# Performance work log

Hardware: AMD Instinct MI355X
Metric: run time of the kernel (lower is better)

## Reference

```python
import jax, jax.numpy as jnp
import numpy as np

MAX_DISP = 4  # max_displacement
PAD = MAX_DISP
ODIM = 2 * MAX_DISP + 1  # 9 -> 81 cost-volume channels


def setup_inputs() -> dict:
    key = jax.random.key(0)
    k1, k2 = jax.random.split(key)
    B, C, H, W = 4, 256, 96, 192
    x1 = jax.random.normal(k1, (B, C, H, W), dtype=jnp.float32)
    x2 = jax.random.normal(k2, (B, C, H, W), dtype=jnp.float32)
    return {"x1": x1, "x2": x2}


def reference(x1, x2):
    B, C, H, W = x1.shape
    # zero-pad x2 spatially by PAD on each side (matches F.pad([pad]*4))
    x2p = jnp.pad(x2, ((0, 0), (0, 0), (PAD, PAD), (PAD, PAD)))
    cv = []
    for i in range(ODIM):          # fixed 9x9 displacement grid
        for j in range(ODIM):
            shifted = jax.lax.dynamic_slice(
                x2p, (0, 0, i, j), (B, C, H, W))
            # mean over channel dim -> [B, H, W]
            cv.append(jnp.mean(x1 * shifted, axis=1))
    return jnp.stack(cv, axis=1)  # [B, 81, H, W]
```

## Files before the change

### kernel.cpp

```cpp
#include <hip/hip_runtime.h>
#include <stddef.h>


#define NB 4
#define NC 256
#define HH 96
#define WW 192
#define TW 16
#define TH 4
#define KC 32
#define NROWS 12
#define CHW (HH * WW)
#define KSTRIDE (KC * CHW)
#define NTASK 1152

#define KS 264
#define RS 1096
#define XBI(row, kg, n) ((row) * RS + (kg) * KS + (n) * 8)

typedef __attribute__((ext_vector_type(8))) short bf16x8;
typedef __attribute__((ext_vector_type(4))) float f32x4;

__device__ __forceinline__ unsigned short f2bf(float f) {
    union { float f; unsigned u; } c; c.f = f;
    unsigned r = c.u + 0x7FFFu + ((c.u >> 16) & 1u);
    return (unsigned short)(r >> 16);
}

__global__ __launch_bounds__(512, 4) void corr_mfma(
    const float* __restrict__ x1, const float* __restrict__ x2,
    float* __restrict__ out)
{
    __shared__ union {
        unsigned short xb[NROWS * RS];
        float band[TH][9][9][18];
    } lds;

    const int lin = blockIdx.x;
    const int sw  = (lin & 7) * 144 + (lin >> 3);
    const int b   = sw / 288;
    const int t2  = sw - b * 288;
    const int ty  = t2 / 12;
    const int tx  = t2 - ty * 12;

    const int tid  = threadIdx.x;
    const int wv   = tid >> 6;
    const int lane = tid & 63;
    const int col  = lane & 15;
    const int q    = lane >> 4;
    const int r    = wv & 3;
    const int dig  = wv >> 2;
    const int w0   = tx * TW;
    const int h0   = ty * TH;
    const int h    = h0 + r;

    f32x4 acc[9];
#pragma unroll
    for (int s = 0; s < 9; ++s) acc[s] = (f32x4)0.0f;

    unsigned o2k[3];
    int      lofk[3];
    bool     okk[3];
    bool     act[3];
#pragma unroll
    for (int k = 0; k < 3; ++k) {
        const int t   = tid + k * 512;
        act[k] = (t < NTASK);
        const int seg = t % 6;
        const int u   = t / 6;
        const int cp  = u & 15;
        const int row = u >> 4;
        const int gh  = h0 - 4 + row;
        const int gw  = w0 - 4 + seg * 4;
        okk[k] = act[k] & (gh >= 0) & (gh < HH) & (gw >= 0) & (gw <= WW - 4);
        const int ghc = gh < 0 ? 0 : (gh > HH - 1 ? HH - 1 : gh);
        const int gwc = gw < 0 ? 0 : gw;
        const int rwc = row > NROWS - 1 ? NROWS - 1 : row;
        o2k[k]  = (unsigned)(((b * NC + cp * 2) * HH + ghc) * WW + gwc);
        lofk[k] = XBI(rwc, cp >> 2, seg * 4) + (cp & 3) * 2;
    }
    unsigned o1 = (unsigned)(((b * NC + q * 8) * HH + h) * WW + w0 + col);

    float pf[24];
    float pa[8];

#define STAGE_LOAD()                                                     \
    {                                                                    \
        _Pragma("unroll")                                                \
        for (int k = 0; k < 3; ++k) {                                    \
            _Pragma("unroll")                                            \
            for (int e = 0; e < 2; ++e) {                                \
                float4 ld = make_float4(0.f, 0.f, 0.f, 0.f);             \
                if (okk[k]) ld = *(const float4*)&x2[o2k[k] + e * CHW];  \
                *(float4*)&pf[(k * 2 + e) * 4] = ld;                     \
            }                                                            \
            o2k[k] += KSTRIDE;                                           \
        }                                                                \
    }

#define X1_LOAD()                                                        \
    {                                                                    \
        _Pragma("unroll")                                                \
        for (int j = 0; j < 8; ++j) pa[j] = x1[o1 + j * CHW];            \
        o1 += KSTRIDE;                                                   \
    }

    STAGE_LOAD();
    X1_LOAD();

    const int rbase = XBI(r, q, col);

    for (int ci = 0; ci < 8; ++ci) {
#pragma unroll
        for (int k = 0; k < 3; ++k) {
            if (act[k]) {
#pragma unroll
                for (int p = 0; p < 4; ++p) {
                    ushort2 v;
                    v.x = f2bf(pf[(k * 2 + 0) * 4 + p]);
                    v.y = f2bf(pf[(k * 2 + 1) * 4 + p]);
                    *(ushort2*)&lds.xb[lofk[k] + p * 8] = v;
                }
            }
        }
        __syncthreads();

        bf16x8 a;
#pragma unroll
        for (int j = 0; j < 8; ++j) a[j] = (short)f2bf(pa[j]);
        if (ci < 7) {
            STAGE_LOAD();
            X1_LOAD();
        }

#pragma unroll
        for (int s = 0; s < 9; ++s) {
            const int u    = dig * 9 + s;
            const int di   = u >> 1;
            const int half = u & 1;
            bf16x8 bb = *(const bf16x8*)&lds.xb[rbase + di * RS + half * 128];
            acc[s] = __builtin_amdgcn_mfma_f32_16x16x32_bf16(a, bb, acc[s], 0, 0, 0);
        }
        __syncthreads();
    }

#pragma unroll
    for (int s = 0; s < 9; ++s) {
        const int u  = dig * 9 + s;
        const int di = u >> 1;
        const int uh = u & 1;
#pragma unroll
        for (int rg = 0; rg < 4; ++rg) {
            int m  = q * 4 + rg;
            int dj = uh * 16 + col - m;
            if (dj >= 0 && dj < 9)
                lds.band[r][di][dj][m] = acc[s][rg];
        }
    }
    __syncthreads();

    const float scale = 1.0f / 256.0f;
#pragma unroll
    for (int it = 0; it < 11; ++it) {
        int gi = it * 32 + (tid >> 4);
        if (gi < 324) {
            int combo = gi >> 2;
            int row   = gi & 3;
            float v = lds.band[row][combo / 9][combo % 9][tid & 15];
            out[((size_t)((b * 81 + combo) * HH + h0 + row)) * WW + w0 + (tid & 15)] = v * scale;
        }
    }
}

extern "C" void kernel_launch(void* const* d_in, const int* in_sizes, int n_in,
                              void* d_out, int out_size, void* d_ws, size_t ws_size,
                              hipStream_t stream) {
    const float* x1 = (const float*)d_in[0];
    const float* x2 = (const float*)d_in[1];
    float* out = (float*)d_out;

    dim3 grid(1152);
    corr_mfma<<<grid, 512, 0, stream>>>(x1, x2, out);
}
```

Measured before the change: 215.2 us.

## Pre-transpose inputs to channel-last bf16 and double-buffer the correlation tiles

```diff
diff --git a/kernel.cpp b/kernel.cpp
--- a/kernel.cpp
+++ b/kernel.cpp
@@ -14,9 +14,12 @@
 #define KSTRIDE (KC * CHW)
 #define NTASK 1152
 
-#define KS 264
-#define RS 1096
-#define XBI(row, kg, n) ((row) * RS + (kg) * KS + (n) * 8)
+#define XT_ELEMS (NB * HH * WW * NC)
+#define XT_BYTES ((size_t)XT_ELEMS * 2)
+
+#define WSTR 36
+#define RSTR (24 * WSTR)
+#define BUFSZ 10688
 
 typedef __attribute__((ext_vector_type(8))) short bf16x8;
 typedef __attribute__((ext_vector_type(4))) float f32x4;
@@ -27,7 +30,169 @@
     return (unsigned short)(r >> 16);
 }
 
-__global__ __launch_bounds__(512, 4) void corr_mfma(
+__global__ __launch_bounds__(256) void transpose_cast(
+    const float* __restrict__ x1, const float* __restrict__ x2,
+    unsigned short* __restrict__ xt1, unsigned short* __restrict__ xt2)
+{
+    __shared__ float t[64][65];
+    int lin = blockIdx.x;
+    const int wt = lin % 3; lin /= 3;
+    const int ct = lin & 3; lin >>= 2;
+    const int h  = lin % 96; lin /= 96;
+    const int b  = lin & 3;  lin >>= 2;
+    const float* __restrict__ src = lin ? x2 : x1;
+    unsigned short* __restrict__ dst = lin ? xt2 : xt1;
+    const int w0 = wt * 64, c0 = ct * 64;
+
+    const int wi = threadIdx.x & 63, c4 = threadIdx.x >> 6;
+#pragma unroll
+    for (int it = 0; it < 16; ++it) {
+        const int c = it * 4 + c4;
+        t[c][wi] = src[((size_t)((b * NC + c0 + c) * HH + h)) * WW + w0 + wi];
+    }
+    __syncthreads();
+    const int co = (threadIdx.x & 31) * 2, wo = threadIdx.x >> 5;
+#pragma unroll
+    for (int it = 0; it < 8; ++it) {
+        const int w = it * 8 + wo;
+        ushort2 v;
+        v.x = f2bf(t[co][w]);
+        v.y = f2bf(t[co + 1][w]);
+        *(ushort2*)&dst[((size_t)((b * HH + h) * WW + w0 + w)) * NC + c0 + co] = v;
+    }
+}
+
+__global__ __launch_bounds__(512, 4) void corr_mfma_bt(
+    const unsigned short* __restrict__ xt1,
+    const unsigned short* __restrict__ xt2,
+    float* __restrict__ out)
+{
+    __shared__ union {
+        unsigned short xb[2 * BUFSZ];
+        float band[TH][9][9][18];
+    } lds;
+
+    const int lin = blockIdx.x;
+    const int sw  = (lin & 7) * 144 + (lin >> 3);
+    const int b   = sw / 288;
+    const int t2  = sw - b * 288;
+    const int ty  = t2 / 12;
+    const int tx  = t2 - ty * 12;
+
+    const int tid  = threadIdx.x;
+    const int wv   = tid >> 6;
+    const int lane = tid & 63;
+    const int col  = lane & 15;
+    const int q    = lane >> 4;
+    const int r    = wv & 3;
+    const int dig  = wv >> 2;
+    const int w0   = tx * TW;
+    const int h0   = ty * TH;
+    const int h    = h0 + r;
+
+    f32x4 acc[9];
+#pragma unroll
+    for (int s = 0; s < 9; ++s) acc[s] = (f32x4)0.0f;
+
+    unsigned go2[3];
+    int      lof[3];
+    bool     okk[3];
+#pragma unroll
+    for (int k = 0; k < 3; ++k) {
+        const int g   = tid + k * 512;
+        const bool act = (g < NTASK);
+        const int row = g / 96;
+        const int rem = g - row * 96;
+        const int w   = rem >> 2;
+        const int sub = rem & 3;
+        const int gh  = h0 - 4 + row;
+        const int gw  = w0 - 4 + w;
+        const bool inb = (gh >= 0) & (gh < HH) & (gw >= 0) & (gw < WW);
+        okk[k] = act & inb;
+        const int ghc = gh < 0 ? 0 : (gh > HH - 1 ? HH - 1 : gh);
+        const int gwc = gw < 0 ? 0 : (gw > WW - 1 ? WW - 1 : gw);
+        const int rwc = row > NROWS - 1 ? NROWS - 1 : row;
+        go2[k] = (unsigned)(((b * HH + ghc) * WW + gwc) * NC + sub * 8);
+        lof[k] = rwc * RSTR + w * WSTR + sub * 8;
+        if (act & !inb) {
+            uint4 z = make_uint4(0, 0, 0, 0);
+            *(uint4*)&lds.xb[lof[k]] = z;
+            *(uint4*)&lds.xb[BUFSZ + lof[k]] = z;
+        }
+    }
+
+    uint4 pfu[3];
+#pragma unroll
+    for (int k = 0; k < 3; ++k) {
+        if (okk[k]) pfu[k] = *(const uint4*)&xt2[go2[k]];
+        go2[k] += KC;
+    }
+    unsigned o1 = (unsigned)(((b * HH + h) * WW + w0 + col) * NC + q * 8);
+    bf16x8 a_cur = *(const bf16x8*)&xt1[o1]; o1 += KC;
+    bf16x8 a_nxt = a_cur;
+
+    const int rb = r * RSTR + q * 8;
+
+#pragma unroll
+    for (int ci = 0; ci < 8; ++ci) {
+        const int pb = (ci & 1) * BUFSZ;
+#pragma unroll
+        for (int k = 0; k < 3; ++k)
+            if (okk[k]) *(uint4*)&lds.xb[pb + lof[k]] = pfu[k];
+        if (ci < 7) {
+#pragma unroll
+            for (int k = 0; k < 3; ++k) {
+                if (okk[k]) pfu[k] = *(const uint4*)&xt2[go2[k]];
+                go2[k] += KC;
+            }
+            a_nxt = *(const bf16x8*)&xt1[o1]; o1 += KC;
+        }
+        __syncthreads();
+#pragma unroll
+        for (int s = 0; s < 9; ++s) {
+            const int u  = dig * 9 + s;
+            const int di = u >> 1;
+            const int n  = (u & 1) * 16 + col;
+            const bf16x8 bb = *(const bf16x8*)&lds.xb[pb + rb + di * RSTR + n * WSTR];
+            acc[s] = __builtin_amdgcn_mfma_f32_16x16x32_bf16(a_cur, bb, acc[s], 0, 0, 0);
+        }
+        a_cur = a_nxt;
+    }
+    __syncthreads();
+
+#pragma unroll
+    for (int s = 0; s < 9; ++s) {
+        const int u  = dig * 9 + s;
+        const int di = u >> 1;
+        const int uh = u & 1;
+#pragma unroll
+        for (int rg = 0; rg < 4; ++rg) {
+            int m  = q * 4 + rg;
+            int dj = uh * 16 + col - m;
+            if (dj >= 0 && dj < 9)
+                lds.band[r][di][dj][m] = acc[s][rg];
+        }
+    }
+    __syncthreads();
+
+    const float scale = 1.0f / 256.0f;
+#pragma unroll
+    for (int it = 0; it < 11; ++it) {
+        int gi = it * 32 + (tid >> 4);
+        if (gi < 324) {
+            int combo = gi >> 2;
+            int row   = gi & 3;
+            float v = lds.band[row][combo / 9][combo % 9][tid & 15];
+            out[((size_t)((b * 81 + combo) * HH + h0 + row)) * WW + w0 + (tid & 15)] = v * scale;
+        }
+    }
+}
+
+#define KS 264
+#define RS 1096
+#define XBI(row, kg, n) ((row) * RS + (kg) * KS + (n) * 8)
+
+__global__ __launch_bounds__(512, 4) void corr_mfma_fb(
     const float* __restrict__ x1, const float* __restrict__ x2,
     float* __restrict__ out)
 {
@@ -84,7 +249,7 @@
     float pf[24];
     float pa[8];
 
-#define STAGE_LOAD()                                                     \
+#define STAGE_LOAD_FB()                                                  \
     {                                                                    \
         _Pragma("unroll")                                                \
         for (int k = 0; k < 3; ++k) {                                    \
@@ -98,15 +263,15 @@
         }                                                                \
     }
 
-#define X1_LOAD()                                                        \
+#define X1_LOAD_FB()                                                     \
     {                                                                    \
         _Pragma("unroll")                                                \
         for (int j = 0; j < 8; ++j) pa[j] = x1[o1 + j * CHW];            \
         o1 += KSTRIDE;                                                   \
     }
 
-    STAGE_LOAD();
-    X1_LOAD();
+    STAGE_LOAD_FB();
+    X1_LOAD_FB();
 
     const int rbase = XBI(r, q, col);
 
@@ -129,8 +294,8 @@
 #pragma unroll
         for (int j = 0; j < 8; ++j) a[j] = (short)f2bf(pa[j]);
         if (ci < 7) {
-            STAGE_LOAD();
-            X1_LOAD();
+            STAGE_LOAD_FB();
+            X1_LOAD_FB();
         }
 
 #pragma unroll
@@ -179,6 +344,12 @@
     const float* x2 = (const float*)d_in[1];
     float* out = (float*)d_out;
 
-    dim3 grid(1152);
-    corr_mfma<<<grid, 512, 0, stream>>>(x1, x2, out);
-}
+    if (ws_size >= 2 * XT_BYTES) {
+        unsigned short* xt1 = (unsigned short*)d_ws;
+        unsigned short* xt2 = xt1 + XT_ELEMS;
+        transpose_cast<<<dim3(9216), 256, 0, stream>>>(x1, x2, xt1, xt2);
+        corr_mfma_bt<<<dim3(1152), 512, 0, stream>>>(xt1, xt2, out);
+    } else {
+        corr_mfma_fb<<<dim3(1152), 512, 0, stream>>>(x1, x2, out);
+    }
+}
```

Result: slower. 261.5 us (+21.5%).
